# Kernel optimization log

Measured on AMD Instinct MI355X. Metric: run time of the kernel, lower is better.

## Reference

```python
import jax, jax.numpy as jnp
import numpy as np

B, C, H, W = 16, 64, 64, 64
HEADS = 8

def conv1x1(x, w):
    # x: [B, Cin, H, W], w: [Cout, Cin] -> [B, Cout, H, W]
    return jnp.einsum('oc,bchw->bohw', w, x)

def maxpool2x2(x):
    b, c, h, w = x.shape
    return x.reshape(b, c, h // 2, 2, w // 2, 2).max(axis=(3, 5))

def setup_inputs() -> dict:
    key = jax.random.key(0)
    ks = jax.random.split(key, 6)
    x = jax.random.normal(ks[0], (B, C, H, W), dtype=jnp.float32)
    w_theta = jax.random.normal(ks[1], (C // HEADS, C), dtype=jnp.float32) * 0.05
    w_phi = jax.random.normal(ks[2], (C // HEADS, C), dtype=jnp.float32) * 0.05
    w_g = jax.random.normal(ks[3], (C // 2, C), dtype=jnp.float32) * 0.05
    w_o = jax.random.normal(ks[4], (C, C // 2), dtype=jnp.float32) * 0.05
    gamma = jax.random.normal(ks[5], (), dtype=jnp.float32)
    return {'x': x, 'w_theta': w_theta, 'w_phi': w_phi, 'w_g': w_g, 'w_o': w_o, 'gamma': gamma}

def reference(x, w_theta, w_phi, w_g, w_o, gamma):
    b, c, h, w = x.shape
    n = h * w                      # query length
    m = n // 4                     # kv length after 2x2 maxpool
    theta = conv1x1(x, w_theta).reshape(b, c // HEADS, n)   # [B, C/h, N]
    phi = maxpool2x2(conv1x1(x, w_phi)).reshape(b, c // HEADS, m)  # [B, C/h, M]
    g = maxpool2x2(conv1x1(x, w_g)).reshape(b, c // 2, m)   # [B, C/2, M]
    # attention: theta^T @ phi -> [B, N, M]; NOTE: no 1/sqrt(d) scaling (SAGAN)
    beta = jax.nn.softmax(jnp.einsum('bdn,bdm->bnm', theta, phi), axis=-1)
    # o = g @ beta^T -> [B, C/2, N]
    o = jnp.einsum('bdm,bnm->bdn', g, beta).reshape(b, c // 2, h, w)
    o = conv1x1(o, w_o)            # [B, C, H, W]
    return gamma * o + x
```

## Files before the change

kernel.cpp:

```cpp
#include <hip/hip_runtime.h>
#include <hip/hip_bf16.h>

#define NB 16
#define NC 64
#define NN 4096
#define NM 1024
#define ND 8
#define NG 32

typedef short short8 __attribute__((ext_vector_type(8)));
typedef float floatx4 __attribute__((ext_vector_type(4)));

#define LOG2E 1.44269504f

__device__ __forceinline__ short f2bfs(float f) {
    union { __hip_bfloat16 h; short s; } u;
    u.h = __float2bfloat16(f);
    return u.s;
}
__device__ __forceinline__ unsigned pack2bf(float a, float b) {
    return (unsigned)(unsigned short)f2bfs(a) | ((unsigned)(unsigned short)f2bfs(b) << 16);
}
__device__ __forceinline__ float bflo(unsigned u) { return __uint_as_float(u << 16); }
__device__ __forceinline__ float bfhi(unsigned u) { return __uint_as_float(u & 0xffff0000u); }

__global__ __launch_bounds__(256)
void proj_kernel(const float* __restrict__ x,
                 const float* __restrict__ w_theta,
                 const float* __restrict__ w_phi,
                 const float* __restrict__ w_g,
                 const float* __restrict__ w_o,
                 unsigned* __restrict__ theta_ws,
                 unsigned* __restrict__ phi_ws,
                 unsigned* __restrict__ g2_ws)
{
    __shared__ __align__(16) float xl[64 * 128];
    __shared__ float lwt[8 * 64];
    __shared__ float lwp[8 * 64];
    __shared__ float lwg[32 * 64];
    __shared__ float lwo[64 * 32];
    __shared__ float lgs[32 * 33];
    __shared__ float lps[32 * 8];

    const int b  = blockIdx.x >> 5;
    const int ph = blockIdx.x & 31;
    const int t  = threadIdx.x;

    for (int i = t; i < 512;  i += 256) { lwt[i] = w_theta[i]; lwp[i] = w_phi[i]; }
    for (int i = t; i < 2048; i += 256) { lwg[i] = w_g[i];     lwo[i] = w_o[i]; }

    const float* xb = x + (size_t)b * NC * NN + (size_t)ph * 128;
    for (int idx = t; idx < 64 * 32; idx += 256) {
        int c = idx >> 5, i4 = idx & 31;
        ((float4*)xl)[idx] = ((const float4*)(xb + (size_t)c * NN))[i4];
    }
    __syncthreads();

    if (t < 128) {
        float th[8];
        #pragma unroll
        for (int oc = 0; oc < 8; ++oc) th[oc] = 0.f;
        for (int c = 0; c < 64; ++c) {
            float xv = xl[c * 128 + t];
            #pragma unroll
            for (int oc = 0; oc < 8; ++oc) th[oc] = fmaf(lwt[oc * 64 + c], xv, th[oc]);
        }
        uint4 pk;
        pk.x = pack2bf(th[0] * LOG2E, th[1] * LOG2E);
        pk.y = pack2bf(th[2] * LOG2E, th[3] * LOG2E);
        pk.z = pack2bf(th[4] * LOG2E, th[5] * LOG2E);
        pk.w = pack2bf(th[6] * LOG2E, th[7] * LOG2E);
        ((uint4*)theta_ws)[(size_t)b * NN + ph * 128 + t] = pk;
    } else {
        int tt = t - 128;
        int m = tt >> 2, oc0 = (tt & 3) * 2;
        float s[2][4];
        #pragma unroll
        for (int a = 0; a < 2; ++a)
            #pragma unroll
            for (int p = 0; p < 4; ++p) s[a][p] = 0.f;
        #pragma unroll 4
        for (int c = 0; c < 64; ++c) {
            const float* xr = &xl[c * 128];
            float x0 = xr[2 * m], x1 = xr[2 * m + 1], x2 = xr[64 + 2 * m], x3 = xr[65 + 2 * m];
            #pragma unroll
            for (int a = 0; a < 2; ++a) {
                float w = lwp[(oc0 + a) * 64 + c];
                s[a][0] = fmaf(w, x0, s[a][0]);
                s[a][1] = fmaf(w, x1, s[a][1]);
                s[a][2] = fmaf(w, x2, s[a][2]);
                s[a][3] = fmaf(w, x3, s[a][3]);
            }
        }
        #pragma unroll
        for (int a = 0; a < 2; ++a)
            lps[m * 8 + oc0 + a] = fmaxf(fmaxf(s[a][0], s[a][1]), fmaxf(s[a][2], s[a][3]));
    }

    for (int idx = t; idx < 32 * 32; idx += 256) {
        int oc = idx >> 5, pw = idx & 31;
        float s0 = 0.f, s1 = 0.f, s2 = 0.f, s3 = 0.f;
        #pragma unroll 4
        for (int c = 0; c < 64; ++c) {
            float w = lwg[oc * 64 + c];
            const float* xr = &xl[c * 128];
            s0 = fmaf(w, xr[2 * pw],      s0);
            s1 = fmaf(w, xr[2 * pw + 1],  s1);
            s2 = fmaf(w, xr[64 + 2 * pw], s2);
            s3 = fmaf(w, xr[65 + 2 * pw], s3);
        }
        lgs[oc * 33 + pw] = fmaxf(fmaxf(s0, s1), fmaxf(s2, s3));
    }
    __syncthreads();

    {
        int co = t >> 2, m0 = (t & 3) * 8;
        float v[8];
        #pragma unroll
        for (int mm = 0; mm < 8; ++mm) v[mm] = 0.f;
        #pragma unroll 4
        for (int c = 0; c < 32; ++c) {
            float w = lwo[co * 32 + c];
            const float* gr = &lgs[c * 33 + m0];
            #pragma unroll
            for (int mm = 0; mm < 8; ++mm) v[mm] = fmaf(w, gr[mm], v[mm]);
        }
        uint4 pk;
        pk.x = pack2bf(v[0], v[1]); pk.y = pack2bf(v[2], v[3]);
        pk.z = pack2bf(v[4], v[5]); pk.w = pack2bf(v[6], v[7]);
        ((uint4*)g2_ws)[(((size_t)b * 64 + co) * NM + ph * 32 + m0) >> 3] = pk;
    }

    if (t < 32) {
        const float* pr = &lps[t * 8];
        uint4 pk;
        pk.x = pack2bf(pr[0], pr[1]); pk.y = pack2bf(pr[2], pr[3]);
        pk.z = pack2bf(pr[4], pr[5]); pk.w = pack2bf(pr[6], pr[7]);
        ((uint4*)phi_ws)[(size_t)b * NM + ph * 32 + t] = pk;
    }
}

__global__ __launch_bounds__(256, 2)
void attn_kernel(const unsigned* __restrict__ theta_ws,
                 const unsigned* __restrict__ phi_ws,
                 const unsigned* __restrict__ g2_ws,
                 const float* __restrict__ gamma_p,
                 const float* __restrict__ x,
                 float* __restrict__ out)
{
    __shared__ __align__(16) float lphi[NM * 8];
    __shared__ __align__(16) uint4 lg2f[2048];

    const int b    = blockIdx.x >> 5;
    const int qblk = blockIdx.x & 31;
    const int t    = threadIdx.x;
    const int w    = t >> 6;
    const int lane = t & 63;
    const int lm   = lane & 15;
    const int quad = lane >> 4;
    const int q0   = qblk * 128 + w * 32;

    for (int kk = t; kk < NM; kk += 256) {
        uint4 v = ((const uint4*)phi_ws)[(size_t)b * NM + kk];
        float4 f0 = make_float4(bflo(v.x), bfhi(v.x), bflo(v.y), bfhi(v.y));
        float4 f1 = make_float4(bflo(v.z), bfhi(v.z), bflo(v.w), bfhi(v.w));
        ((float4*)&lphi[kk * 8])[0] = f0;
        ((float4*)&lphi[kk * 8])[1] = f1;
    }

    float th[2][8];
    #pragma unroll
    for (int qt = 0; qt < 2; ++qt) {
        int q = q0 + qt * 16 + lm;
        uint4 v = ((const uint4*)theta_ws)[(size_t)b * NN + q];
        th[qt][0] = bflo(v.x); th[qt][1] = bfhi(v.x);
        th[qt][2] = bflo(v.y); th[qt][3] = bfhi(v.y);
        th[qt][4] = bflo(v.z); th[qt][5] = bfhi(v.z);
        th[qt][6] = bflo(v.w); th[qt][7] = bfhi(v.w);
    }

    floatx4 acc[2][4];
    #pragma unroll
    for (int qt = 0; qt < 2; ++qt)
        #pragma unroll
        for (int ct = 0; ct < 4; ++ct)
            acc[qt][ct] = (floatx4)0.f;
    float lsum[2] = {0.f, 0.f};

    const int srow = t >> 2;
    const int sseg = t & 3;
    const uint4* gsrc = (const uint4*)g2_ws;

    for (int ch = 0; ch < 4; ++ch) {
        __syncthreads();
        {
            size_t base = ((size_t)b * 64 + srow) * (NM / 8) + ch * 32 + sseg * 8;
            #pragma unroll
            for (int u = 0; u < 8; ++u) {
                uint4 v = gsrc[base + u];
                int kgv = sseg * 2 + (u >> 2);
                int fr = ((srow >> 4) * 8 + kgv) * 64 + ((srow & 15) | ((u & 3) << 4));
                lg2f[fr] = v;
            }
        }
        __syncthreads();

        for (int kg = 0; kg < 8; ++kg) {
            const int kbase = ch * 256 + kg * 32;
            float p[2][8];
            #pragma unroll
            for (int j = 0; j < 8; ++j) {
                int key = kbase + quad * 8 + j;
                const float4* pp = (const float4*)&lphi[key * 8];
                float4 f0 = pp[0], f1 = pp[1];
                #pragma unroll
                for (int qt = 0; qt < 2; ++qt) {
                    float s = th[qt][0] * f0.x;
                    s = fmaf(th[qt][1], f0.y, s); s = fmaf(th[qt][2], f0.z, s);
                    s = fmaf(th[qt][3], f0.w, s); s = fmaf(th[qt][4], f1.x, s);
                    s = fmaf(th[qt][5], f1.y, s); s = fmaf(th[qt][6], f1.z, s);
                    s = fmaf(th[qt][7], f1.w, s);
                    p[qt][j] = exp2f(s);
                }
            }
            short8 pf[2];
            #pragma unroll
            for (int qt = 0; qt < 2; ++qt) {
                float ls = 0.f;
                #pragma unroll
                for (int j = 0; j < 8; ++j) { ls += p[qt][j]; pf[qt][j] = f2bfs(p[qt][j]); }
                lsum[qt] += ls;
            }
            #pragma unroll
            for (int ct = 0; ct < 4; ++ct) {
                uint4 av = lg2f[(ct * 8 + kg) * 64 + lane];
                short8 a2;
                a2[0] = (short)(av.x & 0xffff); a2[1] = (short)(av.x >> 16);
                a2[2] = (short)(av.y & 0xffff); a2[3] = (short)(av.y >> 16);
                a2[4] = (short)(av.z & 0xffff); a2[5] = (short)(av.z >> 16);
                a2[6] = (short)(av.w & 0xffff); a2[7] = (short)(av.w >> 16);
                acc[0][ct] = __builtin_amdgcn_mfma_f32_16x16x32_bf16(a2, pf[0], acc[0][ct], 0, 0, 0);
                acc[1][ct] = __builtin_amdgcn_mfma_f32_16x16x32_bf16(a2, pf[1], acc[1][ct], 0, 0, 0);
            }
        }
    }

    float inv[2];
    #pragma unroll
    for (int qt = 0; qt < 2; ++qt) {
        float l = lsum[qt];
        l += __shfl_xor(l, 16);
        l += __shfl_xor(l, 32);
        inv[qt] = 1.0f / l;
    }

    const float gamma = gamma_p[0];
    #pragma unroll
    for (int qt = 0; qt < 2; ++qt) {
        const int q = q0 + qt * 16 + lm;
        #pragma unroll
        for (int ct = 0; ct < 4; ++ct) {
            #pragma unroll
            for (int r = 0; r < 4; ++r) {
                int co = ct * 16 + quad * 4 + r;
                size_t idx = ((size_t)b * NC + co) * NN + q;
                out[idx] = fmaf(gamma, acc[qt][ct][r] * inv[qt], x[idx]);
            }
        }
    }
}

extern "C" void kernel_launch(void* const* d_in, const int* in_sizes, int n_in,
                              void* d_out, int out_size, void* d_ws, size_t ws_size,
                              hipStream_t stream)
{
    const float* x  = (const float*)d_in[0];
    const float* wt = (const float*)d_in[1];
    const float* wp = (const float*)d_in[2];
    const float* wg = (const float*)d_in[3];
    const float* wo = (const float*)d_in[4];
    const float* gm = (const float*)d_in[5];
    float* out = (float*)d_out;

    unsigned* theta_ws = (unsigned*)d_ws;
    unsigned* phi_ws   = theta_ws + (size_t)NB * NN * ND / 2;
    unsigned* g2_ws    = phi_ws   + (size_t)NB * NM * ND / 2;

    proj_kernel<<<NB * 32, 256, 0, stream>>>(x, wt, wp, wg, wo, theta_ws, phi_ws, g2_ws);
    attn_kernel<<<NB * 32, 256, 0, stream>>>(theta_ws, phi_ws, g2_ws, gm, x, out);
}
```

Measured before the change: 136.3 us.

## Pre-swizzle g2 into MFMA fragment layout and stream it from global with prefetch

The projection kernel now writes g2 directly in the per-lane MFMA A-fragment order, so the attention kernel drops its LDS staging buffer and the per-chunk barriers and instead loads fragments straight from global memory with a one-step register prefetch. The score computation uses packed two-wide float FMAs across the two query tiles, bf16 packing uses a cheap add-and-permute rounding, and the phi LDS layout is padded to reduce bank conflicts. The proj kernel also rebalances work so the g projection uses vectorized LDS reads with more outputs per thread. The gains come from less LDS traffic, fewer syncs and less VALU work, at the cost of global-load latency in the inner loop and slightly different bf16 rounding on ties and NaNs.

```diff
diff --git a/kernel.cpp b/kernel.cpp
--- a/kernel.cpp
+++ b/kernel.cpp
@@ -10,6 +10,7 @@
 
 typedef short short8 __attribute__((ext_vector_type(8)));
 typedef float floatx4 __attribute__((ext_vector_type(4)));
+typedef float floatx2 __attribute__((ext_vector_type(2)));
 
 #define LOG2E 1.44269504f
 
@@ -21,8 +22,16 @@
 __device__ __forceinline__ unsigned pack2bf(float a, float b) {
     return (unsigned)(unsigned short)f2bfs(a) | ((unsigned)(unsigned short)f2bfs(b) << 16);
 }
+__device__ __forceinline__ unsigned pk2fast(float a, float b) {
+    unsigned ua = __float_as_uint(a) + 0x8000u;
+    unsigned ub = __float_as_uint(b) + 0x8000u;
+    return __builtin_amdgcn_perm(ub, ua, 0x07060302);
+}
 __device__ __forceinline__ float bflo(unsigned u) { return __uint_as_float(u << 16); }
 __device__ __forceinline__ float bfhi(unsigned u) { return __uint_as_float(u & 0xffff0000u); }
+__device__ __forceinline__ floatx2 fma2(floatx2 a, float b, floatx2 c) {
+    return __builtin_elementwise_fma(a, (floatx2)(b), c);
+}
 
 __global__ __launch_bounds__(256)
 void proj_kernel(const float* __restrict__ x,
@@ -35,11 +44,11 @@
                  unsigned* __restrict__ g2_ws)
 {
     __shared__ __align__(16) float xl[64 * 128];
-    __shared__ float lwt[8 * 64];
-    __shared__ float lwp[8 * 64];
-    __shared__ float lwg[32 * 64];
-    __shared__ float lwo[64 * 32];
-    __shared__ float lgs[32 * 33];
+    __shared__ float lwt[512];
+    __shared__ float lwp[512];
+    __shared__ float lwg[2048];
+    __shared__ float lwo[2048];
+    __shared__ __align__(16) float lgs[32 * 36];
     __shared__ float lps[32 * 8];
 
     const int b  = blockIdx.x >> 5;
@@ -50,9 +59,9 @@
     for (int i = t; i < 2048; i += 256) { lwg[i] = w_g[i];     lwo[i] = w_o[i]; }
 
     const float* xb = x + (size_t)b * NC * NN + (size_t)ph * 128;
-    for (int idx = t; idx < 64 * 32; idx += 256) {
+    for (int idx = t; idx < 2048; idx += 256) {
         int c = idx >> 5, i4 = idx & 31;
-        ((float4*)xl)[idx] = ((const float4*)(xb + (size_t)c * NN))[i4];
+        ((float4*)xl)[c * 32 + i4] = ((const float4*)(xb + (size_t)c * NN))[i4];
     }
     __syncthreads();
 
@@ -71,9 +80,8 @@
         pk.z = pack2bf(th[4] * LOG2E, th[5] * LOG2E);
         pk.w = pack2bf(th[6] * LOG2E, th[7] * LOG2E);
         ((uint4*)theta_ws)[(size_t)b * NN + ph * 128 + t] = pk;
-    } else {
-        int tt = t - 128;
-        int m = tt >> 2, oc0 = (tt & 3) * 2;
+
+        int m = t >> 2, oc0 = (t & 3) * 2;
         float s[2][4];
         #pragma unroll
         for (int a = 0; a < 2; ++a)
@@ -95,21 +103,44 @@
         #pragma unroll
         for (int a = 0; a < 2; ++a)
             lps[m * 8 + oc0 + a] = fmaxf(fmaxf(s[a][0], s[a][1]), fmaxf(s[a][2], s[a][3]));
-    }
-
-    for (int idx = t; idx < 32 * 32; idx += 256) {
-        int oc = idx >> 5, pw = idx & 31;
-        float s0 = 0.f, s1 = 0.f, s2 = 0.f, s3 = 0.f;
-        #pragma unroll 4
+    } else {
+        int tt = t - 128;
+        int oc0 = (tt >> 3) * 2, grp = tt & 7;
+        float s0[16], s1[16];
+        #pragma unroll
+        for (int i = 0; i < 16; ++i) { s0[i] = 0.f; s1[i] = 0.f; }
+        const float4* xl4 = (const float4*)xl;
+        #pragma unroll 2
         for (int c = 0; c < 64; ++c) {
-            float w = lwg[oc * 64 + c];
-            const float* xr = &xl[c * 128];
-            s0 = fmaf(w, xr[2 * pw],      s0);
-            s1 = fmaf(w, xr[2 * pw + 1],  s1);
-            s2 = fmaf(w, xr[64 + 2 * pw], s2);
-            s3 = fmaf(w, xr[65 + 2 * pw], s3);
-        }
-        lgs[oc * 33 + pw] = fmaxf(fmaxf(s0, s1), fmaxf(s2, s3));
+            float4 a0 = xl4[c * 32 + 2 * grp];
+            float4 a1 = xl4[c * 32 + 2 * grp + 1];
+            float4 b0 = xl4[c * 32 + 16 + 2 * grp];
+            float4 b1 = xl4[c * 32 + 17 + 2 * grp];
+            float w0 = lwg[oc0 * 64 + c], w1 = lwg[(oc0 + 1) * 64 + c];
+            s0[0] = fmaf(w0, a0.x, s0[0]);  s0[1] = fmaf(w0, a0.y, s0[1]);
+            s0[2] = fmaf(w0, a0.z, s0[2]);  s0[3] = fmaf(w0, a0.w, s0[3]);
+            s0[4] = fmaf(w0, a1.x, s0[4]);  s0[5] = fmaf(w0, a1.y, s0[5]);
+            s0[6] = fmaf(w0, a1.z, s0[6]);  s0[7] = fmaf(w0, a1.w, s0[7]);
+            s0[8] = fmaf(w0, b0.x, s0[8]);  s0[9] = fmaf(w0, b0.y, s0[9]);
+            s0[10] = fmaf(w0, b0.z, s0[10]); s0[11] = fmaf(w0, b0.w, s0[11]);
+            s0[12] = fmaf(w0, b1.x, s0[12]); s0[13] = fmaf(w0, b1.y, s0[13]);
+            s0[14] = fmaf(w0, b1.z, s0[14]); s0[15] = fmaf(w0, b1.w, s0[15]);
+            s1[0] = fmaf(w1, a0.x, s1[0]);  s1[1] = fmaf(w1, a0.y, s1[1]);
+            s1[2] = fmaf(w1, a0.z, s1[2]);  s1[3] = fmaf(w1, a0.w, s1[3]);
+            s1[4] = fmaf(w1, a1.x, s1[4]);  s1[5] = fmaf(w1, a1.y, s1[5]);
+            s1[6] = fmaf(w1, a1.z, s1[6]);  s1[7] = fmaf(w1, a1.w, s1[7]);
+            s1[8] = fmaf(w1, b0.x, s1[8]);  s1[9] = fmaf(w1, b0.y, s1[9]);
+            s1[10] = fmaf(w1, b0.z, s1[10]); s1[11] = fmaf(w1, b0.w, s1[11]);
+            s1[12] = fmaf(w1, b1.x, s1[12]); s1[13] = fmaf(w1, b1.y, s1[13]);
+            s1[14] = fmaf(w1, b1.z, s1[14]); s1[15] = fmaf(w1, b1.w, s1[15]);
+        }
+        #pragma unroll
+        for (int p = 0; p < 4; ++p) {
+            float v0 = fmaxf(fmaxf(s0[2 * p], s0[2 * p + 1]), fmaxf(s0[8 + 2 * p], s0[9 + 2 * p]));
+            float v1 = fmaxf(fmaxf(s1[2 * p], s1[2 * p + 1]), fmaxf(s1[8 + 2 * p], s1[9 + 2 * p]));
+            lgs[oc0 * 36 + grp * 4 + p]       = v0;
+            lgs[(oc0 + 1) * 36 + grp * 4 + p] = v1;
+        }
     }
     __syncthreads();
 
@@ -121,14 +152,18 @@
         #pragma unroll 4
         for (int c = 0; c < 32; ++c) {
             float w = lwo[co * 32 + c];
-            const float* gr = &lgs[c * 33 + m0];
-            #pragma unroll
-            for (int mm = 0; mm < 8; ++mm) v[mm] = fmaf(w, gr[mm], v[mm]);
+            float4 ga = ((const float4*)&lgs[c * 36 + m0])[0];
+            float4 gb = ((const float4*)&lgs[c * 36 + m0])[1];
+            v[0] = fmaf(w, ga.x, v[0]); v[1] = fmaf(w, ga.y, v[1]);
+            v[2] = fmaf(w, ga.z, v[2]); v[3] = fmaf(w, ga.w, v[3]);
+            v[4] = fmaf(w, gb.x, v[4]); v[5] = fmaf(w, gb.y, v[5]);
+            v[6] = fmaf(w, gb.z, v[6]); v[7] = fmaf(w, gb.w, v[7]);
         }
         uint4 pk;
         pk.x = pack2bf(v[0], v[1]); pk.y = pack2bf(v[2], v[3]);
         pk.z = pack2bf(v[4], v[5]); pk.w = pack2bf(v[6], v[7]);
-        ((uint4*)g2_ws)[(((size_t)b * 64 + co) * NM + ph * 32 + m0) >> 3] = pk;
+        int lane = ((t & 3) << 4) | ((t >> 2) & 15);
+        ((uint4*)g2_ws)[(((size_t)b * 4 + (t >> 6)) * 32 + ph) * 64 + lane] = pk;
     }
 
     if (t < 32) {
@@ -148,8 +183,7 @@
                  const float* __restrict__ x,
                  float* __restrict__ out)
 {
-    __shared__ __align__(16) float lphi[NM * 8];
-    __shared__ __align__(16) uint4 lg2f[2048];
+    __shared__ __align__(16) float lphi[NM * 8 + 16];
 
     const int b    = blockIdx.x >> 5;
     const int qblk = blockIdx.x & 31;
@@ -162,96 +196,81 @@
 
     for (int kk = t; kk < NM; kk += 256) {
         uint4 v = ((const uint4*)phi_ws)[(size_t)b * NM + kk];
-        float4 f0 = make_float4(bflo(v.x), bfhi(v.x), bflo(v.y), bfhi(v.y));
-        float4 f1 = make_float4(bflo(v.z), bfhi(v.z), bflo(v.w), bfhi(v.w));
-        ((float4*)&lphi[kk * 8])[0] = f0;
-        ((float4*)&lphi[kk * 8])[1] = f1;
-    }
-
-    float th[2][8];
-    #pragma unroll
-    for (int qt = 0; qt < 2; ++qt) {
-        int q = q0 + qt * 16 + lm;
-        uint4 v = ((const uint4*)theta_ws)[(size_t)b * NN + q];
-        th[qt][0] = bflo(v.x); th[qt][1] = bfhi(v.x);
-        th[qt][2] = bflo(v.y); th[qt][3] = bfhi(v.y);
-        th[qt][4] = bflo(v.z); th[qt][5] = bfhi(v.z);
-        th[qt][6] = bflo(v.w); th[qt][7] = bfhi(v.w);
+        float* dst = lphi + kk * 8 + ((kk >> 3) & 3) * 4;
+        ((float4*)dst)[0] = make_float4(bflo(v.x), bfhi(v.x), bflo(v.y), bfhi(v.y));
+        ((float4*)dst)[1] = make_float4(bflo(v.z), bfhi(v.z), bflo(v.w), bfhi(v.w));
+    }
+
+    floatx2 th2[8];
+    {
+        uint4 v0 = ((const uint4*)theta_ws)[(size_t)b * NN + q0 + lm];
+        uint4 v1 = ((const uint4*)theta_ws)[(size_t)b * NN + q0 + 16 + lm];
+        th2[0] = floatx2{bflo(v0.x), bflo(v1.x)}; th2[1] = floatx2{bfhi(v0.x), bfhi(v1.x)};
+        th2[2] = floatx2{bflo(v0.y), bflo(v1.y)}; th2[3] = floatx2{bfhi(v0.y), bfhi(v1.y)};
+        th2[4] = floatx2{bflo(v0.z), bflo(v1.z)}; th2[5] = floatx2{bfhi(v0.z), bfhi(v1.z)};
+        th2[6] = floatx2{bflo(v0.w), bflo(v1.w)}; th2[7] = floatx2{bfhi(v0.w), bfhi(v1.w)};
     }
 
     floatx4 acc[2][4];
     #pragma unroll
     for (int qt = 0; qt < 2; ++qt)
         #pragma unroll
-        for (int ct = 0; ct < 4; ++ct)
-            acc[qt][ct] = (floatx4)0.f;
-    float lsum[2] = {0.f, 0.f};
-
-    const int srow = t >> 2;
-    const int sseg = t & 3;
-    const uint4* gsrc = (const uint4*)g2_ws;
-
-    for (int ch = 0; ch < 4; ++ch) {
-        __syncthreads();
-        {
-            size_t base = ((size_t)b * 64 + srow) * (NM / 8) + ch * 32 + sseg * 8;
-            #pragma unroll
-            for (int u = 0; u < 8; ++u) {
-                uint4 v = gsrc[base + u];
-                int kgv = sseg * 2 + (u >> 2);
-                int fr = ((srow >> 4) * 8 + kgv) * 64 + ((srow & 15) | ((u & 3) << 4));
-                lg2f[fr] = v;
-            }
-        }
-        __syncthreads();
-
-        for (int kg = 0; kg < 8; ++kg) {
-            const int kbase = ch * 256 + kg * 32;
-            float p[2][8];
-            #pragma unroll
-            for (int j = 0; j < 8; ++j) {
-                int key = kbase + quad * 8 + j;
-                const float4* pp = (const float4*)&lphi[key * 8];
-                float4 f0 = pp[0], f1 = pp[1];
-                #pragma unroll
-                for (int qt = 0; qt < 2; ++qt) {
-                    float s = th[qt][0] * f0.x;
-                    s = fmaf(th[qt][1], f0.y, s); s = fmaf(th[qt][2], f0.z, s);
-                    s = fmaf(th[qt][3], f0.w, s); s = fmaf(th[qt][4], f1.x, s);
-                    s = fmaf(th[qt][5], f1.y, s); s = fmaf(th[qt][6], f1.z, s);
-                    s = fmaf(th[qt][7], f1.w, s);
-                    p[qt][j] = exp2f(s);
-                }
-            }
-            short8 pf[2];
-            #pragma unroll
-            for (int qt = 0; qt < 2; ++qt) {
-                float ls = 0.f;
-                #pragma unroll
-                for (int j = 0; j < 8; ++j) { ls += p[qt][j]; pf[qt][j] = f2bfs(p[qt][j]); }
-                lsum[qt] += ls;
-            }
-            #pragma unroll
-            for (int ct = 0; ct < 4; ++ct) {
-                uint4 av = lg2f[(ct * 8 + kg) * 64 + lane];
-                short8 a2;
-                a2[0] = (short)(av.x & 0xffff); a2[1] = (short)(av.x >> 16);
-                a2[2] = (short)(av.y & 0xffff); a2[3] = (short)(av.y >> 16);
-                a2[4] = (short)(av.z & 0xffff); a2[5] = (short)(av.z >> 16);
-                a2[6] = (short)(av.w & 0xffff); a2[7] = (short)(av.w >> 16);
-                acc[0][ct] = __builtin_amdgcn_mfma_f32_16x16x32_bf16(a2, pf[0], acc[0][ct], 0, 0, 0);
-                acc[1][ct] = __builtin_amdgcn_mfma_f32_16x16x32_bf16(a2, pf[1], acc[1][ct], 0, 0, 0);
-            }
-        }
+        for (int ct = 0; ct < 4; ++ct) acc[qt][ct] = (floatx4)0.f;
+    floatx2 lsum2 = (floatx2)0.f;
+
+    const uint4* gf = (const uint4*)g2_ws;
+    uint4 ga[4], gn[4];
+    #pragma unroll
+    for (int ct = 0; ct < 4; ++ct)
+        ga[ct] = gf[(((size_t)b * 4 + ct) * 32 + 0) * 64 + lane];
+
+    __syncthreads();
+
+    for (int kg = 0; kg < 32; ++kg) {
+        if (kg + 1 < 32) {
+            #pragma unroll
+            for (int ct = 0; ct < 4; ++ct)
+                gn[ct] = gf[(((size_t)b * 4 + ct) * 32 + kg + 1) * 64 + lane];
+        }
+        const float* pb = lphi + kg * 256 + quad * 68;
+        floatx2 p2[8];
+        #pragma unroll
+        for (int j = 0; j < 8; ++j) {
+            float4 f0 = ((const float4*)(pb + j * 8))[0];
+            float4 f1 = ((const float4*)(pb + j * 8))[1];
+            floatx2 s2 = th2[0] * f0.x;
+            s2 = fma2(th2[1], f0.y, s2); s2 = fma2(th2[2], f0.z, s2);
+            s2 = fma2(th2[3], f0.w, s2); s2 = fma2(th2[4], f1.x, s2);
+            s2 = fma2(th2[5], f1.y, s2); s2 = fma2(th2[6], f1.z, s2);
+            s2 = fma2(th2[7], f1.w, s2);
+            floatx2 e2;
+            e2.x = exp2f(s2.x);
+            e2.y = exp2f(s2.y);
+            lsum2 += e2;
+            p2[j] = e2;
+        }
+        union { unsigned u[4]; short8 s; } pf0, pf1;
+        #pragma unroll
+        for (int jj = 0; jj < 4; ++jj) {
+            pf0.u[jj] = pk2fast(p2[2 * jj].x, p2[2 * jj + 1].x);
+            pf1.u[jj] = pk2fast(p2[2 * jj].y, p2[2 * jj + 1].y);
+        }
+        #pragma unroll
+        for (int ct = 0; ct < 4; ++ct) {
+            union { uint4 v; short8 s; } a;
+            a.v = ga[ct];
+            acc[0][ct] = __builtin_amdgcn_mfma_f32_16x16x32_bf16(a.s, pf0.s, acc[0][ct], 0, 0, 0);
+            acc[1][ct] = __builtin_amdgcn_mfma_f32_16x16x32_bf16(a.s, pf1.s, acc[1][ct], 0, 0, 0);
+        }
+        #pragma unroll
+        for (int ct = 0; ct < 4; ++ct) ga[ct] = gn[ct];
     }
 
     float inv[2];
-    #pragma unroll
-    for (int qt = 0; qt < 2; ++qt) {
-        float l = lsum[qt];
-        l += __shfl_xor(l, 16);
-        l += __shfl_xor(l, 32);
-        inv[qt] = 1.0f / l;
+    {
+        float l0 = lsum2.x; l0 += __shfl_xor(l0, 16); l0 += __shfl_xor(l0, 32);
+        float l1 = lsum2.y; l1 += __shfl_xor(l1, 16); l1 += __shfl_xor(l1, 32);
+        inv[0] = 1.0f / l0; inv[1] = 1.0f / l1;
     }
 
     const float gamma = gamma_p[0];
```

Measured after the change: 128.5 us. 1.06x faster.
